# Performance work log

Measured on AMD Instinct MI355X. Metric: run time of the kernel, lower is better.

The kernel has to match this reference:

```python
import jax, jax.numpy as jnp
import numpy as np

B, L, M, H = 8, 256, 128, 768


def setup_inputs() -> dict:
    key = jax.random.key(0)
    ks = jax.random.split(key, 12)
    s = 1.0 / np.sqrt(H)
    sa = 1.0 / np.sqrt(2 * H)
    return {
        "text_features": jax.random.normal(ks[0], (B, L, H), jnp.float32),
        "dns_features": jax.random.normal(ks[1], (B, M, H), jnp.float32),
        # block 1 params (text_linear_1 has bias, dns_linear_1 no bias, att_linear_1: 2H->1)
        "W_t1": jax.random.uniform(ks[2], (H, H), jnp.float32, -s, s),
        "b_t1": jax.random.uniform(ks[3], (H,), jnp.float32, -s, s),
        "W_d1": jax.random.uniform(ks[4], (H, H), jnp.float32, -s, s),
        "w_att1": jax.random.uniform(ks[5], (2 * H,), jnp.float32, -sa, sa),
        "b_att1": jax.random.uniform(ks[6], (), jnp.float32, -sa, sa),
        # block 2 params (dns_linear_2 has bias, text_linear_2 no bias, att_linear_2: 2H->1)
        "W_d2": jax.random.uniform(ks[7], (H, H), jnp.float32, -s, s),
        "b_d2": jax.random.uniform(ks[8], (H,), jnp.float32, -s, s),
        "W_t2": jax.random.uniform(ks[9], (H, H), jnp.float32, -s, s),
        "w_att2": jax.random.uniform(ks[10], (2 * H,), jnp.float32, -sa, sa),
        "b_att2": jax.random.uniform(ks[11], (), jnp.float32, -sa, sa),
    }


def reference(text_features, dns_features, W_t1, b_t1, W_d1, w_att1, b_att1,
              W_d2, b_d2, W_t2, w_att2, b_att2):
    # Block 1: additive co-attention text -> dns.
    # tanh(cat([Lin(text_rep), Lin(dns_rep)])) @ w_att1 decomposes because tanh is
    # elementwise on the concat and the 2H->1 linear splits into two H-dot-products.
    t1 = jnp.tanh(jnp.einsum('blh,oh->blo', text_features, W_t1) + b_t1)  # (B,L,H)
    d1 = jnp.tanh(jnp.einsum('bmh,oh->bmo', dns_features, W_d1))          # (B,M,H)
    wa, wb = w_att1[:H], w_att1[H:]
    score1 = (t1 @ wa)[:, :, None] + (d1 @ wb)[:, None, :] + b_att1       # (B,L,M)
    a1 = jax.nn.softmax(score1, axis=-1)
    att_dns = jnp.einsum('blm,bmh->blh', a1, dns_features)                # (B,L,H)

    # Block 2: additive co-attention dns-context -> text.
    d2 = jnp.tanh(jnp.einsum('blh,oh->blo', att_dns, W_d2) + b_d2)        # (B,L,H)
    t2 = jnp.tanh(jnp.einsum('bjh,oh->bjo', text_features, W_t2))         # (B,L,H)
    wc, wd = w_att2[:H], w_att2[H:]
    score2 = (d2 @ wc)[:, :, None] + (t2 @ wd)[:, None, :] + b_att2       # (B,L,L)
    a2 = jax.nn.softmax(score2, axis=-1)
    att_text = jnp.einsum('blj,bjh->blh', a2, text_features)              # (B,L,H)

    return (att_text, att_dns)
```

## Files before the change

### kernel.cpp

```cpp
#include <hip/hip_runtime.h>
#include <hip/hip_bf16.h>
#include <math.h>

#define HH 768
#define NB 8
#define LL 256
#define MM 128
#define NROW1 (NB*MM)
#define NROW2 (NB*LL)
#define NROWS (NROW1+NROW2)
#define NCB 12

typedef __attribute__((ext_vector_type(8))) short  bf16x8;
typedef __attribute__((ext_vector_type(4))) float  f32x4;

static __device__ __forceinline__ unsigned int pkbf2(float a, float b) {
    __hip_bfloat162 h = __float22bfloat162_rn(make_float2(a, b));
    unsigned int u; __builtin_memcpy(&u, &h, 4); return u;
}

static __device__ __forceinline__ float fast_tanh(float x) {
    float e = __expf(2.0f * x);
    return 1.0f - 2.0f * __builtin_amdgcn_rcpf(e + 1.0f);
}

__global__ __launch_bounds__(256) void prep_bf16(
    const float4* __restrict__ text, const float4* __restrict__ dns,
    const float4* __restrict__ Wd1, const float4* __restrict__ Wt2,
    uint2* __restrict__ Xb, uint2* __restrict__ Wb)
{
    const int i = blockIdx.x * 256 + threadIdx.x;
    const float4* src; uint2* dst;
    if (i < 589824) {
        dst = Xb + i;
        src = (i < 196608) ? (dns + i) : (text + (i - 196608));
    } else {
        dst = Wb + (i - 589824);
        src = (i < 737280) ? (Wd1 + (i - 589824)) : (Wt2 + (i - 737280));
    }
    float4 v = *src;
    uint2 o; o.x = pkbf2(v.x, v.y); o.y = pkbf2(v.z, v.w);
    *dst = o;
}

__global__ __launch_bounds__(256) void score_mfma(
    const unsigned short* __restrict__ Xb, const unsigned short* __restrict__ Wb,
    const float* __restrict__ wv1, const float* __restrict__ wv2,
    float* __restrict__ partial)
{
    __shared__ __align__(16) unsigned short As[64][72];
    __shared__ __align__(16) unsigned short Bs[64][72];

    const int t = threadIdx.x;
    const int tile = (blockIdx.x >> 3) + (blockIdx.x & 7) * 72;
    const int rb = tile / 12, cb = tile % 12;
    const int row0 = rb * 64, col0 = cb * 64;

    const unsigned short* X = Xb + (size_t)row0 * HH;
    const unsigned short* W; const float* wv;
    if (row0 < NROW1) { W = Wb;                    wv = wv1; }
    else              { W = Wb + (size_t)HH * HH;  wv = wv2; }

    const int sr = t >> 2;
    const int c4 = t & 3;
    const unsigned short* xp = X + (size_t)sr * HH + c4 * 16;
    const unsigned short* wp = W + (size_t)(col0 + sr) * HH + c4 * 16;

    const int l  = t & 63;
    const int w  = t >> 6;
    const int wr = w * 16;
    const int lc = l & 15;
    const int lk = (l >> 4) * 8;

    f32x4 acc[4] = {};
    uint4 rA0, rA1, rB0, rB1, nA0, nA1, nB0, nB1;

    auto STAGE = [&]() {
        *reinterpret_cast<uint4*>(&As[sr][c4 * 16    ]) = rA0;
        *reinterpret_cast<uint4*>(&As[sr][c4 * 16 + 8]) = rA1;
        *reinterpret_cast<uint4*>(&Bs[sr][c4 * 16    ]) = rB0;
        *reinterpret_cast<uint4*>(&Bs[sr][c4 * 16 + 8]) = rB1;
    };
    auto MFMA_TILE = [&]() {
        #pragma unroll
        for (int kk = 0; kk < 2; ++kk) {
            const int ko = kk * 32 + lk;
            bf16x8 a = *reinterpret_cast<const bf16x8*>(&As[wr + lc][ko]);
            #pragma unroll
            for (int n = 0; n < 4; ++n) {
                bf16x8 b = *reinterpret_cast<const bf16x8*>(&Bs[n*16 + lc][ko]);
                acc[n] = __builtin_amdgcn_mfma_f32_16x16x32_bf16(a, b, acc[n], 0, 0, 0);
            }
        }
    };

    rA0 = *(const uint4*)(xp);     rA1 = *(const uint4*)(xp + 8);
    rB0 = *(const uint4*)(wp);     rB1 = *(const uint4*)(wp + 8);

    #pragma unroll 1
    for (int k0 = 0; k0 < HH - 64; k0 += 64) {
        STAGE();
        __syncthreads();
        nA0 = *(const uint4*)(xp + k0 + 64);  nA1 = *(const uint4*)(xp + k0 + 72);
        nB0 = *(const uint4*)(wp + k0 + 64);  nB1 = *(const uint4*)(wp + k0 + 72);
        MFMA_TILE();
        __syncthreads();
        rA0 = nA0; rA1 = nA1; rB0 = nB0; rB1 = nB1;
    }
    STAGE();
    __syncthreads();
    MFMA_TILE();

    float wvn[4];
    #pragma unroll
    for (int n = 0; n < 4; ++n) wvn[n] = wv[col0 + n*16 + lc];
    #pragma unroll
    for (int i = 0; i < 4; ++i) {
        float s = 0.f;
        #pragma unroll
        for (int n = 0; n < 4; ++n) s += fast_tanh(acc[n][i]) * wvn[n];
        s += __shfl_xor(s, 1);
        s += __shfl_xor(s, 2);
        s += __shfl_xor(s, 4);
        s += __shfl_xor(s, 8);
        if (lc == 0)
            partial[(size_t)(row0 + wr + (l >> 4)*4 + i) * NCB + cb] = s;
    }
}

__global__ __launch_bounds__(256) void tail_kernel(
    const float* __restrict__ text, const float* __restrict__ dns,
    const float* __restrict__ partial, float* __restrict__ out)
{
    const int b = blockIdx.x, hc = blockIdx.y;
    const int t = threadIdx.x;
    __shared__ float p1s[128], p2s[256], red[8];
    __shared__ __align__(16) float bt[256], bd[256];

    if (t < 128) {
        const float* pr = partial + (size_t)(b * MM + t) * NCB;
        float s = 0.f;
        #pragma unroll
        for (int c = 0; c < NCB; ++c) s += pr[c];
        p1s[t] = s;
    }
    {
        const float* pr = partial + (size_t)(NROW1 + b * LL + t) * NCB;
        float s = 0.f;
        #pragma unroll
        for (int c = 0; c < NCB; ++c) s += pr[c];
        p2s[t] = s;
    }
    __syncthreads();

    float x1 = (t < 128) ? p1s[t] : -1e30f;
    float m1 = x1;
    #pragma unroll
    for (int d = 1; d < 64; d <<= 1) m1 = fmaxf(m1, __shfl_xor(m1, d));
    if ((t & 63) == 0) red[t >> 6] = m1;
    float x2 = p2s[t];
    float m2 = x2;
    #pragma unroll
    for (int d = 1; d < 64; d <<= 1) m2 = fmaxf(m2, __shfl_xor(m2, d));
    if ((t & 63) == 0) red[4 + (t >> 6)] = m2;
    __syncthreads();
    m1 = fmaxf(fmaxf(red[0], red[1]), fmaxf(red[2], red[3]));
    m2 = fmaxf(fmaxf(red[4], red[5]), fmaxf(red[6], red[7]));

    float e1 = (t < 128) ? __expf(x1 - m1) : 0.f;
    float e2 = __expf(x2 - m2);
    __syncthreads();
    float s1 = e1, s2 = e2;
    #pragma unroll
    for (int d = 1; d < 64; d <<= 1) { s1 += __shfl_xor(s1, d); s2 += __shfl_xor(s2, d); }
    if ((t & 63) == 0) { red[t >> 6] = s1; red[4 + (t >> 6)] = s2; }
    __syncthreads();
    s1 = red[0] + red[1] + red[2] + red[3];
    s2 = red[4] + red[5] + red[6] + red[7];
    if (t < 128) p1s[t] = e1 / s1;
    p2s[t] = e2 / s2;
    __syncthreads();

    const int hh  = hc * 16 + (t & 15);
    const int rsl = t >> 4;

    const int jr0 = rsl * 16;
    float st = 0.f;
    #pragma unroll
    for (int r = 0; r < 16; ++r)
        st = fmaf(p2s[jr0 + r], text[(size_t)(b * LL + jr0 + r) * HH + hh], st);

    const int mr0 = rsl * 8;
    float sd = 0.f;
    #pragma unroll
    for (int r = 0; r < 8; ++r)
        sd = fmaf(p1s[mr0 + r], dns[(size_t)(b * MM + mr0 + r) * HH + hh], sd);

    bt[t] = st; bd[t] = sd;
    __syncthreads();
    if (t < 128) { bt[t] += bt[t + 128]; bd[t] += bd[t + 128]; } __syncthreads();
    if (t < 64)  { bt[t] += bt[t + 64];  bd[t] += bd[t + 64];  } __syncthreads();
    if (t < 32)  { bt[t] += bt[t + 32];  bd[t] += bd[t + 32];  } __syncthreads();
    if (t < 16)  { bt[t] += bt[t + 16];  bd[t] += bd[t + 16];  }
    __syncthreads();

    const int H4 = HH / 4;
    const int n4out = NB * LL * H4;
    const float4* svt4 = reinterpret_cast<const float4*>(bt);
    const float4* svd4 = reinterpret_cast<const float4*>(bd);
    float4* out4 = reinterpret_cast<float4*>(out);
    #pragma unroll
    for (int i = t; i < LL * 4; i += 256) {
        const int ll = i >> 2, c4 = i & 3;
        const size_t o = (size_t)(b * LL + ll) * H4 + hc * 4 + c4;
        out4[o] = svt4[c4];
        out4[n4out + o] = svd4[c4];
    }
}

extern "C" void kernel_launch(void* const* d_in, const int* in_sizes, int n_in,
                              void* d_out, int out_size, void* d_ws, size_t ws_size,
                              hipStream_t stream) {
    const float* text   = (const float*)d_in[0];
    const float* dns    = (const float*)d_in[1];
    const float* W_d1   = (const float*)d_in[4];
    const float* w_att1 = (const float*)d_in[5];
    const float* W_t2   = (const float*)d_in[9];
    const float* w_att2 = (const float*)d_in[10];

    float* ws      = (float*)d_ws;
    float* partial = ws;
    unsigned short* Xb = (unsigned short*)(ws + 36864);
    unsigned short* Wb = Xb + (size_t)NROWS * HH;
    float* out     = (float*)d_out;

    prep_bf16<<<3456, 256, 0, stream>>>(
        (const float4*)text, (const float4*)dns, (const float4*)W_d1,
        (const float4*)W_t2, (uint2*)Xb, (uint2*)Wb);
    score_mfma<<<576, 256, 0, stream>>>(
        Xb, Wb, w_att1 + HH, w_att2 + HH, partial);
    tail_kernel<<<dim3(NB, 48), 256, 0, stream>>>(text, dns, partial, out);
}
```

Measured before the change: 30.71 us.

## Load MFMA operands directly from global memory with triple-buffered registers

The score GEMM kernel stops staging A and B tiles through shared memory. Each lane now loads its MFMA fragments straight from global/L2 into registers, using a three-stage register rotation to prefetch ahead, and all __syncthreads barriers in the K loop are gone. In exchange, B rows are fetched redundantly by all four waves and A without coalesced staging, so global/L2 traffic and register pressure rise.

```diff
diff --git a/kernel.cpp b/kernel.cpp
--- a/kernel.cpp
+++ b/kernel.cpp
@@ -48,9 +48,6 @@
     const float* __restrict__ wv1, const float* __restrict__ wv2,
     float* __restrict__ partial)
 {
-    __shared__ __align__(16) unsigned short As[64][72];
-    __shared__ __align__(16) unsigned short Bs[64][72];
-
     const int t = threadIdx.x;
     const int tile = (blockIdx.x >> 3) + (blockIdx.x & 7) * 72;
     const int rb = tile / 12, cb = tile % 12;
@@ -60,11 +57,6 @@
     const unsigned short* W; const float* wv;
     if (row0 < NROW1) { W = Wb;                    wv = wv1; }
     else              { W = Wb + (size_t)HH * HH;  wv = wv2; }
-
-    const int sr = t >> 2;
-    const int c4 = t & 3;
-    const unsigned short* xp = X + (size_t)sr * HH + c4 * 16;
-    const unsigned short* wp = W + (size_t)(col0 + sr) * HH + c4 * 16;
 
     const int l  = t & 63;
     const int w  = t >> 6;
@@ -72,44 +64,44 @@
     const int lc = l & 15;
     const int lk = (l >> 4) * 8;
 
+    const unsigned short* ap = X + (size_t)(wr + lc) * HH + lk;
+    const unsigned short* bp = W + (size_t)(col0 + lc) * HH + lk;
+    const size_t bn = (size_t)16 * HH;
+
     f32x4 acc[4] = {};
-    uint4 rA0, rA1, rB0, rB1, nA0, nA1, nB0, nB1;
-
-    auto STAGE = [&]() {
-        *reinterpret_cast<uint4*>(&As[sr][c4 * 16    ]) = rA0;
-        *reinterpret_cast<uint4*>(&As[sr][c4 * 16 + 8]) = rA1;
-        *reinterpret_cast<uint4*>(&Bs[sr][c4 * 16    ]) = rB0;
-        *reinterpret_cast<uint4*>(&Bs[sr][c4 * 16 + 8]) = rB1;
+
+    uint4 a0, b00, b01, b02, b03;
+    uint4 a1, b10, b11, b12, b13;
+    uint4 a2, b20, b21, b22, b23;
+
+    auto LD = [&](uint4& A, uint4& B0, uint4& B1, uint4& B2, uint4& B3, int s) {
+        const int ko = s * 32;
+        A  = *(const uint4*)(ap + ko);
+        B0 = *(const uint4*)(bp + ko);
+        B1 = *(const uint4*)(bp + bn + ko);
+        B2 = *(const uint4*)(bp + 2 * bn + ko);
+        B3 = *(const uint4*)(bp + 3 * bn + ko);
     };
-    auto MFMA_TILE = [&]() {
-        #pragma unroll
-        for (int kk = 0; kk < 2; ++kk) {
-            const int ko = kk * 32 + lk;
-            bf16x8 a = *reinterpret_cast<const bf16x8*>(&As[wr + lc][ko]);
-            #pragma unroll
-            for (int n = 0; n < 4; ++n) {
-                bf16x8 b = *reinterpret_cast<const bf16x8*>(&Bs[n*16 + lc][ko]);
-                acc[n] = __builtin_amdgcn_mfma_f32_16x16x32_bf16(a, b, acc[n], 0, 0, 0);
-            }
-        }
+    auto MF = [&](uint4& A, uint4& B0, uint4& B1, uint4& B2, uint4& B3) {
+        bf16x8 a = *reinterpret_cast<const bf16x8*>(&A);
+        acc[0] = __builtin_amdgcn_mfma_f32_16x16x32_bf16(a, *(const bf16x8*)&B0, acc[0], 0, 0, 0);
+        acc[1] = __builtin_amdgcn_mfma_f32_16x16x32_bf16(a, *(const bf16x8*)&B1, acc[1], 0, 0, 0);
+        acc[2] = __builtin_amdgcn_mfma_f32_16x16x32_bf16(a, *(const bf16x8*)&B2, acc[2], 0, 0, 0);
+        acc[3] = __builtin_amdgcn_mfma_f32_16x16x32_bf16(a, *(const bf16x8*)&B3, acc[3], 0, 0, 0);
     };
 
-    rA0 = *(const uint4*)(xp);     rA1 = *(const uint4*)(xp + 8);
-    rB0 = *(const uint4*)(wp);     rB1 = *(const uint4*)(wp + 8);
+    LD(a0, b00, b01, b02, b03, 0);
+    LD(a1, b10, b11, b12, b13, 1);
 
     #pragma unroll 1
-    for (int k0 = 0; k0 < HH - 64; k0 += 64) {
-        STAGE();
-        __syncthreads();
-        nA0 = *(const uint4*)(xp + k0 + 64);  nA1 = *(const uint4*)(xp + k0 + 72);
-        nB0 = *(const uint4*)(wp + k0 + 64);  nB1 = *(const uint4*)(wp + k0 + 72);
-        MFMA_TILE();
-        __syncthreads();
-        rA0 = nA0; rA1 = nA1; rB0 = nB0; rB1 = nB1;
-    }
-    STAGE();
-    __syncthreads();
-    MFMA_TILE();
+    for (int s = 0; s < 24; s += 3) {
+        LD(a2, b20, b21, b22, b23, s + 2);
+        MF(a0, b00, b01, b02, b03);
+        LD(a0, b00, b01, b02, b03, (s + 3 < 24) ? s + 3 : 23);
+        MF(a1, b10, b11, b12, b13);
+        LD(a1, b10, b11, b12, b13, (s + 4 < 24) ? s + 4 : 23);
+        MF(a2, b20, b21, b22, b23);
+    }
 
     float wvn[4];
     #pragma unroll
```

After: 60.68 us. 1.98x slower.

## Use direct global-to-LDS loads with double buffering and XOR swizzle in score GEMM

Applied to the files above, without the earlier changes.

Replaces the register-staged global loads plus LDS stores in the score GEMM with global_load_lds direct-to-LDS transfers into two ping-pong buffers. An XOR swizzle on 16-byte chunks replaces row padding to avoid LDS bank conflicts. The loop now needs one barrier per k-step instead of two, and the next tile's load overlaps the current MFMAs. Correctness depends on the wave-uniform LDS base plus per-lane 16-byte layout matching the swizzled read indexing, and on the barrier being enough to ensure the async LDS writes have completed.

```diff
diff --git a/kernel.cpp b/kernel.cpp
--- a/kernel.cpp
+++ b/kernel.cpp
@@ -22,6 +22,12 @@
 static __device__ __forceinline__ float fast_tanh(float x) {
     float e = __expf(2.0f * x);
     return 1.0f - 2.0f * __builtin_amdgcn_rcpf(e + 1.0f);
+}
+
+static __device__ __forceinline__ void gload_lds16(const void* g, void* l) {
+    __builtin_amdgcn_global_load_lds(
+        (const __attribute__((address_space(1))) unsigned int*)g,
+        (__attribute__((address_space(3))) unsigned int*)l, 16, 0, 0);
 }
 
 __global__ __launch_bounds__(256) void prep_bf16(
@@ -48,8 +54,8 @@
     const float* __restrict__ wv1, const float* __restrict__ wv2,
     float* __restrict__ partial)
 {
-    __shared__ __align__(16) unsigned short As[64][72];
-    __shared__ __align__(16) unsigned short Bs[64][72];
+    __shared__ __align__(16) unsigned short A2[2][64 * 64];
+    __shared__ __align__(16) unsigned short B2[2][64 * 64];
 
     const int t = threadIdx.x;
     const int tile = (blockIdx.x >> 3) + (blockIdx.x & 7) * 72;
@@ -60,11 +66,6 @@
     const unsigned short* W; const float* wv;
     if (row0 < NROW1) { W = Wb;                    wv = wv1; }
     else              { W = Wb + (size_t)HH * HH;  wv = wv2; }
-
-    const int sr = t >> 2;
-    const int c4 = t & 3;
-    const unsigned short* xp = X + (size_t)sr * HH + c4 * 16;
-    const unsigned short* wp = W + (size_t)(col0 + sr) * HH + c4 * 16;
 
     const int l  = t & 63;
     const int w  = t >> 6;
@@ -72,44 +73,48 @@
     const int lc = l & 15;
     const int lk = (l >> 4) * 8;
 
+    const int roff = l >> 3;
+    const int gch  = ((l & 7) ^ roff) * 8;
+    const int rA0  = w * 16 + roff;
+    const unsigned short* apx = X + (size_t)rA0 * HH + gch;
+    const unsigned short* bpx = W + (size_t)(col0 + rA0) * HH + gch;
+
     f32x4 acc[4] = {};
-    uint4 rA0, rA1, rB0, rB1, nA0, nA1, nB0, nB1;
-
-    auto STAGE = [&]() {
-        *reinterpret_cast<uint4*>(&As[sr][c4 * 16    ]) = rA0;
-        *reinterpret_cast<uint4*>(&As[sr][c4 * 16 + 8]) = rA1;
-        *reinterpret_cast<uint4*>(&Bs[sr][c4 * 16    ]) = rB0;
-        *reinterpret_cast<uint4*>(&Bs[sr][c4 * 16 + 8]) = rB1;
+
+    auto STAGE = [&](int buf, int k0) {
+        unsigned short* Abase = &A2[buf][(w * 16) * 64];
+        unsigned short* Bbase = &B2[buf][(w * 16) * 64];
+        gload_lds16(apx + k0,            Abase);
+        gload_lds16(apx + 8 * HH + k0,   Abase + 8 * 64);
+        gload_lds16(bpx + k0,            Bbase);
+        gload_lds16(bpx + 8 * HH + k0,   Bbase + 8 * 64);
     };
-    auto MFMA_TILE = [&]() {
+
+    auto MFMA_TILE = [&](int buf) {
         #pragma unroll
         for (int kk = 0; kk < 2; ++kk) {
-            const int ko = kk * 32 + lk;
-            bf16x8 a = *reinterpret_cast<const bf16x8*>(&As[wr + lc][ko]);
+            const int C = kk * 4 + (l >> 4);
+            const int sw = (C ^ (lc & 7)) * 8;
+            bf16x8 a = *reinterpret_cast<const bf16x8*>(&A2[buf][(wr + lc) * 64 + sw]);
             #pragma unroll
             for (int n = 0; n < 4; ++n) {
-                bf16x8 b = *reinterpret_cast<const bf16x8*>(&Bs[n*16 + lc][ko]);
+                bf16x8 b = *reinterpret_cast<const bf16x8*>(&B2[buf][(n * 16 + lc) * 64 + sw]);
                 acc[n] = __builtin_amdgcn_mfma_f32_16x16x32_bf16(a, b, acc[n], 0, 0, 0);
             }
         }
     };
 
-    rA0 = *(const uint4*)(xp);     rA1 = *(const uint4*)(xp + 8);
-    rB0 = *(const uint4*)(wp);     rB1 = *(const uint4*)(wp + 8);
-
+    STAGE(0, 0);
+    __syncthreads();
+
+    int buf = 0;
     #pragma unroll 1
-    for (int k0 = 0; k0 < HH - 64; k0 += 64) {
-        STAGE();
+    for (int k0 = 0; k0 < HH; k0 += 64) {
+        if (k0 + 64 < HH) STAGE(buf ^ 1, k0 + 64);
+        MFMA_TILE(buf);
         __syncthreads();
-        nA0 = *(const uint4*)(xp + k0 + 64);  nA1 = *(const uint4*)(xp + k0 + 72);
-        nB0 = *(const uint4*)(wp + k0 + 64);  nB1 = *(const uint4*)(wp + k0 + 72);
-        MFMA_TILE();
-        __syncthreads();
-        rA0 = nA0; rA1 = nA1; rB0 = nB0; rB1 = nB1;
-    }
-    STAGE();
-    __syncthreads();
-    MFMA_TILE();
+        buf ^= 1;
+    }
 
     float wvn[4];
     #pragma unroll
```

Result: faster. 29.63 us (-3.5%).
